# Kernel tuning notes

Measured on AMD Instinct MI355X. Metric: run time of the kernel, lower is better.

The kernel has to match this reference:

```python
import jax, jax.numpy as jnp
import numpy as np

HIDDEN = 512
N_HEAD = 8
D_HEAD = 64
MAX_REL = 3
B, S = 2, 2048


def setup_inputs() -> dict:
    key = jax.random.key(0)
    ks = jax.random.split(key, 12)
    sc = 1.0 / np.sqrt(HIDDEN)
    return {
        "query": jax.random.normal(ks[0], (B, S, HIDDEN), jnp.float32),
        "key_": jax.random.normal(ks[1], (B, S, HIDDEN), jnp.float32),
        "value": jax.random.normal(ks[2], (B, S, HIDDEN), jnp.float32),
        "mask": jnp.zeros((B, S, S), dtype=bool),
        "pos_matrix": jax.random.randint(ks[3], (S, S), 0, MAX_REL, jnp.int32),
        "Wq": jax.random.normal(ks[4], (HIDDEN, HIDDEN), jnp.float32) * sc,
        "bq": jnp.zeros((HIDDEN,), jnp.float32),
        "Wk": jax.random.normal(ks[5], (HIDDEN, HIDDEN), jnp.float32) * sc,
        "bk": jnp.zeros((HIDDEN,), jnp.float32),
        "Wv": jax.random.normal(ks[6], (HIDDEN, HIDDEN), jnp.float32) * sc,
        "bv": jnp.zeros((HIDDEN,), jnp.float32),
        "Wo": jax.random.normal(ks[7], (HIDDEN, HIDDEN), jnp.float32) * sc,
        "bo": jnp.zeros((HIDDEN,), jnp.float32),
        "rel_table": jax.random.normal(ks[8], (MAX_REL, D_HEAD), jnp.float32) * 0.1,
    }


def reference(query, key_, value, mask, pos_matrix, Wq, bq, Wk, bk, Wv, bv, Wo, bo, rel_table):
    b, s, hid = query.shape
    H, D = N_HEAD, D_HEAD
    q = (query @ Wq + bq).reshape(b, s, H, D)   # [B,S,H,D]
    k = (key_ @ Wk + bk).reshape(b, s, H, D)
    v = (value @ Wv + bv).reshape(b, s, H, D)
    rel = rel_table[pos_matrix[:s, :s]]          # [S,S,D]
    # attn1: content-content; attn2: q vs rel-pos; attn3: k(row) vs rel-pos
    attn1 = jnp.einsum('bihd,bjhd->bhij', q, k)
    attn2 = jnp.einsum('bihd,ijd->bhij', q, rel)
    attn3 = jnp.einsum('bihd,ijd->bhij', k, rel)
    scale = jnp.sqrt(jnp.asarray(D, query.dtype))
    attn = (attn1 + attn2 + attn3) / scale
    attn = jnp.where(mask[:, None, :, :], jnp.asarray(-1e9, attn.dtype), attn)
    attn = jax.nn.softmax(attn, axis=-1)         # dropout=0 (eval)
    x = jnp.einsum('bhij,bjhd->bihd', attn, v).reshape(b, s, hid)
    out = x @ Wo + bo
    return out, attn
```

## Files before the change

kernel.cpp:

```cpp
#include <hip/hip_runtime.h>
#include <math.h>

#define SEQ   2048
#define BATCH 2
#define NHEAD 8
#define HID   512
#define LG8   0.180336880f
#define MASKV -3.0e8f

typedef unsigned char  u8;
typedef unsigned short u16;
typedef short short8 __attribute__((ext_vector_type(8)));
typedef float f32x4  __attribute__((ext_vector_type(4)));

__device__ __forceinline__ u16 f2bf(float f) {
    unsigned u = __float_as_uint(f);
    u = (u + 0x7FFF + ((u >> 16) & 1)) >> 16;
    return (u16)u;
}
__device__ __forceinline__ float bf2f(u16 h) {
    return __uint_as_float(((unsigned)h) << 16);
}

__global__ __launch_bounds__(256) void prep_w_kernel(
    const float* __restrict__ W, u16* __restrict__ Wth, u16* __restrict__ Wtl)
{
    __shared__ float Ws[64][68];
    const int tid = threadIdx.x;
    const int k0 = blockIdx.x << 6;
    const int n0 = blockIdx.y << 6;
    const int rr = tid >> 2, c4 = (tid & 3) << 4;
    #pragma unroll
    for (int e = 0; e < 4; ++e) {
        float4 v = *(const float4*)&W[(size_t)(k0 + rr) * HID + n0 + c4 + (e << 2)];
        *(float4*)&Ws[rr][c4 + (e << 2)] = v;
    }
    __syncthreads();
    const int nn = tid >> 2, kk = (tid & 3) << 4;
    u16 hb[16], lb[16];
    #pragma unroll
    for (int e = 0; e < 16; ++e) {
        float x = Ws[kk + e][nn];
        u16 hi = f2bf(x);
        hb[e] = hi;
        lb[e] = f2bf(x - bf2f(hi));
    }
    const size_t o = (size_t)(n0 + nn) * HID + k0 + kk;
    *(short8*)&Wth[o]     = *(short8*)&hb[0];
    *(short8*)&Wth[o + 8] = *(short8*)&hb[8];
    *(short8*)&Wtl[o]     = *(short8*)&lb[0];
    *(short8*)&Wtl[o + 8] = *(short8*)&lb[8];
}

__global__ __launch_bounds__(256) void convert_split_kernel(
    const float* __restrict__ src, u16* __restrict__ h, u16* __restrict__ l)
{
    const size_t i = ((size_t)blockIdx.x * 256 + threadIdx.x) * 4;
    float4 v = *(const float4*)&src[i];
    ushort4 oh, ol; u16 hh;
    hh = f2bf(v.x); oh.x = hh; ol.x = f2bf(v.x - bf2f(hh));
    hh = f2bf(v.y); oh.y = hh; ol.y = f2bf(v.y - bf2f(hh));
    hh = f2bf(v.z); oh.z = hh; ol.z = f2bf(v.z - bf2f(hh));
    hh = f2bf(v.w); oh.w = hh; ol.w = f2bf(v.w - bf2f(hh));
    *(ushort4*)&h[i] = oh; *(ushort4*)&l[i] = ol;
}

template<int MODE>
__global__ __launch_bounds__(256) void gemm_mfma_kernel(
    const u16* __restrict__ Ah, const u16* __restrict__ Al,
    const u16* __restrict__ Wth, const u16* __restrict__ Wtl,
    const float* __restrict__ bias,
    float* __restrict__ Cf, u16* __restrict__ Oh, u16* __restrict__ Ol)
{
    __shared__ __align__(16) u16 Sa_h[64 * 72];
    __shared__ __align__(16) u16 Sa_l[64 * 72];
    __shared__ __align__(16) u16 Sw_h[64 * 72];
    __shared__ __align__(16) u16 Sw_l[64 * 72];
    const int tid = threadIdx.x;
    const int wave = tid >> 6, lane = tid & 63;
    const int quad = lane >> 4, l15 = lane & 15;
    const int row0 = blockIdx.x << 6, col0 = blockIdx.y << 6;
    const int rr = tid >> 2, cc = (tid & 3) << 4;

    const size_t ga = (size_t)(row0 + rr) * HID + cc;
    const size_t gw = (size_t)(col0 + rr) * HID + cc;

    f32x4 acc[4] = {{0.f,0.f,0.f,0.f},{0.f,0.f,0.f,0.f},{0.f,0.f,0.f,0.f},{0.f,0.f,0.f,0.f}};

    for (int k0 = 0; k0 < HID; k0 += 64) {
        const short8 ah0 = *(const short8*)&Ah[ga + k0];
        const short8 ah1 = *(const short8*)&Ah[ga + k0 + 8];
        const short8 al0 = *(const short8*)&Al[ga + k0];
        const short8 al1 = *(const short8*)&Al[ga + k0 + 8];
        const short8 wh0 = *(const short8*)&Wth[gw + k0];
        const short8 wh1 = *(const short8*)&Wth[gw + k0 + 8];
        const short8 wl0 = *(const short8*)&Wtl[gw + k0];
        const short8 wl1 = *(const short8*)&Wtl[gw + k0 + 8];
        __syncthreads();
        *(short8*)&Sa_h[rr * 72 + cc]     = ah0;
        *(short8*)&Sa_h[rr * 72 + cc + 8] = ah1;
        *(short8*)&Sa_l[rr * 72 + cc]     = al0;
        *(short8*)&Sa_l[rr * 72 + cc + 8] = al1;
        *(short8*)&Sw_h[rr * 72 + cc]     = wh0;
        *(short8*)&Sw_h[rr * 72 + cc + 8] = wh1;
        *(short8*)&Sw_l[rr * 72 + cc]     = wl0;
        *(short8*)&Sw_l[rr * 72 + cc + 8] = wl1;
        __syncthreads();
        #pragma unroll
        for (int s = 0; s < 2; ++s) {
            const int ao = ((wave << 4) + l15) * 72 + (s << 5) + (quad << 3);
            const short8 fa_h = *(const short8*)&Sa_h[ao];
            const short8 fa_l = *(const short8*)&Sa_l[ao];
            #pragma unroll
            for (int nt = 0; nt < 4; ++nt) {
                const int bo = ((nt << 4) + l15) * 72 + (s << 5) + (quad << 3);
                const short8 fb_h = *(const short8*)&Sw_h[bo];
                const short8 fb_l = *(const short8*)&Sw_l[bo];
                acc[nt] = __builtin_amdgcn_mfma_f32_16x16x32_bf16(fa_h, fb_h, acc[nt], 0, 0, 0);
                acc[nt] = __builtin_amdgcn_mfma_f32_16x16x32_bf16(fa_l, fb_h, acc[nt], 0, 0, 0);
                acc[nt] = __builtin_amdgcn_mfma_f32_16x16x32_bf16(fa_h, fb_l, acc[nt], 0, 0, 0);
            }
        }
    }
    #pragma unroll
    for (int nt = 0; nt < 4; ++nt) {
        const int col = col0 + (nt << 4) + l15;
        const float bv = bias[col];
        #pragma unroll
        for (int r = 0; r < 4; ++r) {
            const size_t row = (size_t)(row0 + (wave << 4) + (quad << 2) + r);
            const float v = acc[nt][r] + bv;
            if constexpr (MODE == 0) {
                Cf[row * HID + col] = v;
            } else if constexpr (MODE == 1) {
                const float sv = v * LG8;
                const u16 hi = f2bf(sv);
                Oh[row * HID + col] = hi;
                Ol[row * HID + col] = f2bf(sv - bf2f(hi));
            } else if constexpr (MODE == 2) {
                const u16 hi = f2bf(v);
                Oh[row * HID + col] = hi;
                Ol[row * HID + col] = f2bf(v - bf2f(hi));
            } else {
                Oh[row * HID + col] = f2bf(v);
            }
        }
    }
}

__global__ __launch_bounds__(256) void convert_pm_kernel(
    const int* __restrict__ pos, const u8* __restrict__ mask, u8* __restrict__ pm)
{
    const size_t s = ((size_t)blockIdx.x * 256 + threadIdx.x) * 4;
    int4  p = *(const int4*)&pos[s & (size_t)(SEQ * SEQ - 1)];
    uchar4 m = *(const uchar4*)&mask[s];
    uchar4 o;
    o.x = m.x ? (u8)3 : (u8)p.x;
    o.y = m.y ? (u8)3 : (u8)p.y;
    o.z = m.z ? (u8)3 : (u8)p.z;
    o.w = m.w ? (u8)3 : (u8)p.w;
    *(uchar4*)&pm[s] = o;
}

__global__ __launch_bounds__(256) void rel_dots_kernel(
    const u16* __restrict__ qh, const u16* __restrict__ ql,
    const u16* __restrict__ kh, const u16* __restrict__ kl,
    const float* __restrict__ rel_table, float* __restrict__ dqk)
{
    const int w = blockIdx.x * 4 + (threadIdx.x >> 6);
    const int lane = threadIdx.x & 63;
    const int h = w % NHEAD;
    const int is = w / NHEAD;
    const int b = is / SEQ;
    const int i = is % SEQ;
    const size_t base = (size_t)is * HID + h * 64 + lane;
    const float qs = bf2f(qh[base]) + bf2f(ql[base]);
    const float kv = bf2f(kh[base]) + bf2f(kl[base]);
    const float s = qs + LG8 * kv;
    float p0 = s * rel_table[lane];
    float p1 = s * rel_table[64 + lane];
    float p2 = s * rel_table[128 + lane];
    #pragma unroll
    for (int off = 32; off; off >>= 1) {
        p0 += __shfl_xor(p0, off);
        p1 += __shfl_xor(p1, off);
        p2 += __shfl_xor(p2, off);
    }
    if (lane == 0) {
        size_t o = (((size_t)b * NHEAD + h) * SEQ + i) << 2;
        dqk[o + 0] = p0; dqk[o + 1] = p1; dqk[o + 2] = p2;
    }
}

__global__ __launch_bounds__(256) void attn_stats_kernel(
    const u16* __restrict__ qh, const u16* __restrict__ ql,
    const u16* __restrict__ kh, const u16* __restrict__ kl,
    const float* __restrict__ dqk, const u8* __restrict__ pm,
    float* __restrict__ invl)
{
    __shared__ __align__(16) u16 Kh[64 * 72];
    __shared__ __align__(16) u16 Kl[64 * 72];
    __shared__ __align__(16) u8  PM[64 * 64];
    __shared__ float Ds[64][4];
    const int tid = threadIdx.x;
    const int wave = tid >> 6, lane = tid & 63;
    const int quad = lane >> 4, l15 = lane & 15;
    const int b = blockIdx.z, h = blockIdx.y, i0 = blockIdx.x << 6;
    const size_t bh = (size_t)(b * NHEAD + h);

    {
        const int i = tid >> 2, r = tid & 3;
        Ds[i][r] = (r == 3) ? MASKV : dqk[((bh * SEQ + i0 + i) << 2) + r];
    }
    const int irow = (wave << 4) + l15;
    const size_t qbase = ((size_t)(b * SEQ + i0 + irow)) * HID + h * 64 + (quad << 3);
    const short8 aqh0 = *(const short8*)&qh[qbase];
    const short8 aqh1 = *(const short8*)&qh[qbase + 32];
    const short8 aql0 = *(const short8*)&ql[qbase];
    const short8 aql1 = *(const short8*)&ql[qbase + 32];

    float srow[4] = {0.f, 0.f, 0.f, 0.f};

    for (int jt = 0; jt < SEQ / 64; ++jt) {
        const int j0 = jt << 6;
        __syncthreads();
        {
            const int rr = tid >> 3, cc = (tid & 7) << 3;
            const size_t g = ((size_t)(b * SEQ + j0 + rr)) * HID + h * 64 + cc;
            *(short8*)&Kh[rr * 72 + cc] = *(const short8*)&kh[g];
            *(short8*)&Kl[rr * 72 + cc] = *(const short8*)&kl[g];
            const size_t g2 = g + (size_t)32 * HID;
            *(short8*)&Kh[(rr + 32) * 72 + cc] = *(const short8*)&kh[g2];
            *(short8*)&Kl[(rr + 32) * 72 + cc] = *(const short8*)&kl[g2];
        }
        {
            const int r = tid >> 2, c = (tid & 3) << 4;
            *(uint4*)&PM[r * 64 + c] =
                *(const uint4*)&pm[((size_t)b * SEQ + i0 + r) * SEQ + j0 + c];
        }
        __syncthreads();

        #pragma unroll
        for (int sub = 0; sub < 4; ++sub) {
            const int n = (sub << 4) + l15;
            const short8 bh0 = *(const short8*)&Kh[n * 72 + (quad << 3)];
            const short8 bh1 = *(const short8*)&Kh[n * 72 + 32 + (quad << 3)];
            const short8 bl0 = *(const short8*)&Kl[n * 72 + (quad << 3)];
            const short8 bl1 = *(const short8*)&Kl[n * 72 + 32 + (quad << 3)];
            f32x4 acc = {0.f, 0.f, 0.f, 0.f};
            acc = __builtin_amdgcn_mfma_f32_16x16x32_bf16(aqh0, bh0, acc, 0, 0, 0);
            acc = __builtin_amdgcn_mfma_f32_16x16x32_bf16(aqh1, bh1, acc, 0, 0, 0);
            acc = __builtin_amdgcn_mfma_f32_16x16x32_bf16(aql0, bh0, acc, 0, 0, 0);
            acc = __builtin_amdgcn_mfma_f32_16x16x32_bf16(aql1, bh1, acc, 0, 0, 0);
            acc = __builtin_amdgcn_mfma_f32_16x16x32_bf16(aqh0, bl0, acc, 0, 0, 0);
            acc = __builtin_amdgcn_mfma_f32_16x16x32_bf16(aqh1, bl1, acc, 0, 0, 0);
            #pragma unroll
            for (int r = 0; r < 4; ++r) {
                const int il = (wave << 4) + (quad << 2) + r;
                const u8 p = PM[il * 64 + (sub << 4) + l15];
                srow[r] += exp2f(acc[r] + Ds[il][p]);
            }
        }
    }
    #pragma unroll
    for (int r = 0; r < 4; ++r) {
        float s = srow[r];
        s += __shfl_xor(s, 1); s += __shfl_xor(s, 2);
        s += __shfl_xor(s, 4); s += __shfl_xor(s, 8);
        if (l15 == 0)
            invl[bh * SEQ + i0 + (wave << 4) + (quad << 2) + r] = 1.0f / s;
    }
}

__global__ __launch_bounds__(256) void attn_fused_kernel(
    const u16* __restrict__ qh, const u16* __restrict__ ql,
    const u16* __restrict__ kh, const u16* __restrict__ kl,
    const u16* __restrict__ vb, const float* __restrict__ dqk,
    const u8* __restrict__ pm, const float* __restrict__ invl,
    float* __restrict__ attn, float* __restrict__ x)
{
    __shared__ __align__(16) u16 Kh[64 * 72];
    __shared__ __align__(16) u16 Kl[64 * 72];
    __shared__ __align__(16) u16 VtT[64 * 72];
    __shared__ __align__(16) u16 Pst[4][16 * 72];
    __shared__ __align__(16) u8  PM[64 * 64];
    __shared__ float Ds[64][4];
    const int tid = threadIdx.x;
    const int wave = tid >> 6, lane = tid & 63;
    const int quad = lane >> 4, l15 = lane & 15;
    const int b = blockIdx.z, h = blockIdx.y, i0 = blockIdx.x << 6;
    const size_t bh = (size_t)(b * NHEAD + h);

    {
        const int i = tid >> 2, r = tid & 3;
        Ds[i][r] = (r == 3) ? MASKV : dqk[((bh * SEQ + i0 + i) << 2) + r];
    }
    float inv_r[4];
    #pragma unroll
    for (int r = 0; r < 4; ++r)
        inv_r[r] = invl[bh * SEQ + i0 + (wave << 4) + (quad << 2) + r];

    const int irow = (wave << 4) + l15;
    const size_t qbase = ((size_t)(b * SEQ + i0 + irow)) * HID + h * 64 + (quad << 3);
    const short8 aqh0 = *(const short8*)&qh[qbase];
    const short8 aqh1 = *(const short8*)&qh[qbase + 32];
    const short8 aql0 = *(const short8*)&ql[qbase];
    const short8 aql1 = *(const short8*)&ql[qbase + 32];

    f32x4 accX[4] = {{0.f,0.f,0.f,0.f},{0.f,0.f,0.f,0.f},{0.f,0.f,0.f,0.f},{0.f,0.f,0.f,0.f}};

    for (int jt = 0; jt < SEQ / 64; ++jt) {
        const int j0 = jt << 6;
        __syncthreads();
        {
            const int rr = tid >> 3, cc = (tid & 7) << 3;
            const size_t g = ((size_t)(b * SEQ + j0 + rr)) * HID + h * 64 + cc;
            *(short8*)&Kh[rr * 72 + cc] = *(const short8*)&kh[g];
            *(short8*)&Kl[rr * 72 + cc] = *(const short8*)&kl[g];
            const size_t g2 = g + (size_t)32 * HID;
            *(short8*)&Kh[(rr + 32) * 72 + cc] = *(const short8*)&kh[g2];
            *(short8*)&Kl[(rr + 32) * 72 + cc] = *(const short8*)&kl[g2];
        }
        {
            const int r = tid >> 2, c = (tid & 3) << 4;
            *(uint4*)&PM[r * 64 + c] =
                *(const uint4*)&pm[((size_t)b * SEQ + i0 + r) * SEQ + j0 + c];
        }
        {
            const int jr = tid & 63, d0 = (tid >> 6) << 4;
            const size_t g = ((size_t)(b * SEQ + j0 + jr)) * HID + h * 64 + d0;
            const short8 v0 = *(const short8*)&vb[g];
            const short8 v1 = *(const short8*)&vb[g + 8];
            #pragma unroll
            for (int e = 0; e < 8; ++e) {
                VtT[(d0 + e) * 72 + jr]     = (u16)v0[e];
                VtT[(d0 + 8 + e) * 72 + jr] = (u16)v1[e];
            }
        }
        __syncthreads();

        #pragma unroll
        for (int sub = 0; sub < 4; ++sub) {
            const int n = (sub << 4) + l15;
            const short8 bh0 = *(const short8*)&Kh[n * 72 + (quad << 3)];
            const short8 bh1 = *(const short8*)&Kh[n * 72 + 32 + (quad << 3)];
            const short8 bl0 = *(const short8*)&Kl[n * 72 + (quad << 3)];
            const short8 bl1 = *(const short8*)&Kl[n * 72 + 32 + (quad << 3)];
            f32x4 acc = {0.f, 0.f, 0.f, 0.f};
            acc = __builtin_amdgcn_mfma_f32_16x16x32_bf16(aqh0, bh0, acc, 0, 0, 0);
            acc = __builtin_amdgcn_mfma_f32_16x16x32_bf16(aqh1, bh1, acc, 0, 0, 0);
            acc = __builtin_amdgcn_mfma_f32_16x16x32_bf16(aql0, bh0, acc, 0, 0, 0);
            acc = __builtin_amdgcn_mfma_f32_16x16x32_bf16(aql1, bh1, acc, 0, 0, 0);
            acc = __builtin_amdgcn_mfma_f32_16x16x32_bf16(aqh0, bl0, acc, 0, 0, 0);
            acc = __builtin_amdgcn_mfma_f32_16x16x32_bf16(aqh1, bl1, acc, 0, 0, 0);
            #pragma unroll
            for (int r = 0; r < 4; ++r) {
                const int il = (wave << 4) + (quad << 2) + r;
                const u8 p = PM[il * 64 + (sub << 4) + l15];
                const float pr = exp2f(acc[r] + Ds[il][p]) * inv_r[r];
                attn[(bh * SEQ + i0 + il) * SEQ + j0 + (sub << 4) + l15] = pr;
                Pst[wave][((quad << 2) + r) * 72 + (sub << 4) + l15] = f2bf(pr);
            }
        }
        const short8 bp0 = *(const short8*)&Pst[wave][l15 * 72 + (quad << 3)];
        const short8 bp1 = *(const short8*)&Pst[wave][l15 * 72 + 32 + (quad << 3)];
        #pragma unroll
        for (int m = 0; m < 4; ++m) {
            const short8 av0 = *(const short8*)&VtT[((m << 4) + l15) * 72 + (quad << 3)];
            const short8 av1 = *(const short8*)&VtT[((m << 4) + l15) * 72 + 32 + (quad << 3)];
            accX[m] = __builtin_amdgcn_mfma_f32_16x16x32_bf16(av0, bp0, accX[m], 0, 0, 0);
            accX[m] = __builtin_amdgcn_mfma_f32_16x16x32_bf16(av1, bp1, accX[m], 0, 0, 0);
        }
    }
    const size_t xrow = ((size_t)(b * SEQ + i0 + (wave << 4) + l15)) * HID + h * 64;
    #pragma unroll
    for (int m = 0; m < 4; ++m) {
        *(f32x4*)&x[xrow + (m << 4) + (quad << 2)] = accX[m];
    }
}

extern "C" void kernel_launch(void* const* d_in, const int* in_sizes, int n_in,
                              void* d_out, int out_size, void* d_ws, size_t ws_size,
                              hipStream_t stream) {
    (void)in_sizes; (void)n_in; (void)out_size; (void)ws_size;
    const float* query = (const float*)d_in[0];
    const float* key_  = (const float*)d_in[1];
    const float* value = (const float*)d_in[2];
    const u8*    mask  = (const u8*)d_in[3];
    const int*   pos   = (const int*)d_in[4];
    const float* Wq = (const float*)d_in[5];
    const float* bq = (const float*)d_in[6];
    const float* Wk = (const float*)d_in[7];
    const float* bk = (const float*)d_in[8];
    const float* Wv = (const float*)d_in[9];
    const float* bv = (const float*)d_in[10];
    const float* Wo = (const float*)d_in[11];
    const float* bo = (const float*)d_in[12];
    const float* rel_table = (const float*)d_in[13];

    float* out  = (float*)d_out;
    float* attn = out + (size_t)BATCH * SEQ * HID;

    u16* qh = (u16*)d_ws;
    u16* ql = qh + (size_t)2097152;
    u16* kh = ql + (size_t)2097152;
    u16* kl = kh + (size_t)2097152;
    u16* vb = kl + (size_t)2097152;
    float* dqk  = (float*)(vb + (size_t)2097152);
    float* invl = dqk + (size_t)131072;
    u8*  pm  = (u8*)(invl + (size_t)32768);
    float* x_ws = (float*)(pm + (size_t)8388608);
    u16* bufAh = (u16*)(x_ws + (size_t)2097152);
    u16* bufAl = bufAh + (size_t)2097152;
    u16* Wth = bufAl + (size_t)2097152;
    u16* Wtl = Wth + (size_t)262144;

    const dim3 blk(256);
    const dim3 gemm_grid(64, 8);
    const dim3 prep_grid(8, 8);

    prep_w_kernel<<<prep_grid, blk, 0, stream>>>(Wq, Wth, Wtl);
    convert_split_kernel<<<dim3(2048), blk, 0, stream>>>(query, bufAh, bufAl);
    gemm_mfma_kernel<1><<<gemm_grid, blk, 0, stream>>>(bufAh, bufAl, Wth, Wtl, bq,
                                                       nullptr, qh, ql);
    prep_w_kernel<<<prep_grid, blk, 0, stream>>>(Wk, Wth, Wtl);
    convert_split_kernel<<<dim3(2048), blk, 0, stream>>>(key_, bufAh, bufAl);
    gemm_mfma_kernel<2><<<gemm_grid, blk, 0, stream>>>(bufAh, bufAl, Wth, Wtl, bk,
                                                       nullptr, kh, kl);
    prep_w_kernel<<<prep_grid, blk, 0, stream>>>(Wv, Wth, Wtl);
    convert_split_kernel<<<dim3(2048), blk, 0, stream>>>(value, bufAh, bufAl);
    gemm_mfma_kernel<3><<<gemm_grid, blk, 0, stream>>>(bufAh, bufAl, Wth, Wtl, bv,
                                                       nullptr, vb, nullptr);

    rel_dots_kernel<<<dim3(BATCH * SEQ * NHEAD / 4), blk, 0, stream>>>(
        qh, ql, kh, kl, rel_table, dqk);
    convert_pm_kernel<<<dim3(8192), blk, 0, stream>>>(pos, mask, pm);
    attn_stats_kernel<<<dim3(SEQ / 64, NHEAD, BATCH), blk, 0, stream>>>(
        qh, ql, kh, kl, dqk, pm, invl);
    attn_fused_kernel<<<dim3(SEQ / 64, NHEAD, BATCH), blk, 0, stream>>>(
        qh, ql, kh, kl, vb, dqk, pm, invl, attn, x_ws);

    prep_w_kernel<<<prep_grid, blk, 0, stream>>>(Wo, Wth, Wtl);
    convert_split_kernel<<<dim3(2048), blk, 0, stream>>>(x_ws, bufAh, bufAl);
    gemm_mfma_kernel<0><<<gemm_grid, blk, 0, stream>>>(bufAh, bufAl, Wth, Wtl, bo,
                                                       out, nullptr, nullptr);
}
```

Baseline: 596.6 us.

## Fuse activation bf16 split into GEMMs and batch weight/mask prep launches

Drops the separate convert_split passes by converting fp32 activations to hi/lo bf16 inside the GEMM tile load, merges the four weight-prep launches and the pos/mask conversion into one kernel, and runs the Q/K/V projections as a single launch using a z grid dimension. This cuts the kernel launch count and removes the intermediate bf16 activation buffers and their write/read traffic. In exchange, each GEMM block loads twice the activation bytes in fp32 and does the split arithmetic per tile, and the mode selection becomes a runtime branch on blockIdx.z.

```diff
diff --git a/kernel.cpp b/kernel.cpp
--- a/kernel.cpp
+++ b/kernel.cpp
@@ -22,60 +22,77 @@
     return __uint_as_float(((unsigned)h) << 16);
 }
 
-__global__ __launch_bounds__(256) void prep_w_kernel(
-    const float* __restrict__ W, u16* __restrict__ Wth, u16* __restrict__ Wtl)
+__global__ __launch_bounds__(256) void misc_prep_kernel(
+    const float* __restrict__ Wq, const float* __restrict__ Wk,
+    const float* __restrict__ Wv, const float* __restrict__ Wo,
+    u16* __restrict__ Wth, u16* __restrict__ Wtl,
+    const int* __restrict__ pos, const u8* __restrict__ mask, u8* __restrict__ pm)
 {
     __shared__ float Ws[64][68];
     const int tid = threadIdx.x;
-    const int k0 = blockIdx.x << 6;
-    const int n0 = blockIdx.y << 6;
-    const int rr = tid >> 2, c4 = (tid & 3) << 4;
-    #pragma unroll
-    for (int e = 0; e < 4; ++e) {
-        float4 v = *(const float4*)&W[(size_t)(k0 + rr) * HID + n0 + c4 + (e << 2)];
-        *(float4*)&Ws[rr][c4 + (e << 2)] = v;
-    }
-    __syncthreads();
-    const int nn = tid >> 2, kk = (tid & 3) << 4;
-    u16 hb[16], lb[16];
-    #pragma unroll
-    for (int e = 0; e < 16; ++e) {
-        float x = Ws[kk + e][nn];
-        u16 hi = f2bf(x);
-        hb[e] = hi;
-        lb[e] = f2bf(x - bf2f(hi));
-    }
-    const size_t o = (size_t)(n0 + nn) * HID + k0 + kk;
-    *(short8*)&Wth[o]     = *(short8*)&hb[0];
-    *(short8*)&Wth[o + 8] = *(short8*)&hb[8];
-    *(short8*)&Wtl[o]     = *(short8*)&lb[0];
-    *(short8*)&Wtl[o + 8] = *(short8*)&lb[8];
-}
-
-__global__ __launch_bounds__(256) void convert_split_kernel(
-    const float* __restrict__ src, u16* __restrict__ h, u16* __restrict__ l)
-{
-    const size_t i = ((size_t)blockIdx.x * 256 + threadIdx.x) * 4;
-    float4 v = *(const float4*)&src[i];
-    ushort4 oh, ol; u16 hh;
-    hh = f2bf(v.x); oh.x = hh; ol.x = f2bf(v.x - bf2f(hh));
-    hh = f2bf(v.y); oh.y = hh; ol.y = f2bf(v.y - bf2f(hh));
-    hh = f2bf(v.z); oh.z = hh; ol.z = f2bf(v.z - bf2f(hh));
-    hh = f2bf(v.w); oh.w = hh; ol.w = f2bf(v.w - bf2f(hh));
-    *(ushort4*)&h[i] = oh; *(ushort4*)&l[i] = ol;
-}
-
-template<int MODE>
-__global__ __launch_bounds__(256) void gemm_mfma_kernel(
-    const u16* __restrict__ Ah, const u16* __restrict__ Al,
-    const u16* __restrict__ Wth, const u16* __restrict__ Wtl,
-    const float* __restrict__ bias,
-    float* __restrict__ Cf, u16* __restrict__ Oh, u16* __restrict__ Ol)
+    const int bid = blockIdx.x;
+    if (bid < 256) {
+        const int w = bid >> 6, sub = bid & 63;
+        const float* W = (w == 0) ? Wq : (w == 1) ? Wk : (w == 2) ? Wv : Wo;
+        u16* oth = Wth + (size_t)w * 262144;
+        u16* otl = Wtl + (size_t)w * 262144;
+        const int k0 = (sub & 7) << 6;
+        const int n0 = (sub >> 3) << 6;
+        const int rr = tid >> 2, c4 = (tid & 3) << 4;
+        #pragma unroll
+        for (int e = 0; e < 4; ++e) {
+            float4 v = *(const float4*)&W[(size_t)(k0 + rr) * HID + n0 + c4 + (e << 2)];
+            *(float4*)&Ws[rr][c4 + (e << 2)] = v;
+        }
+        __syncthreads();
+        const int nn = tid >> 2, kk = (tid & 3) << 4;
+        u16 hb[16], lb[16];
+        #pragma unroll
+        for (int e = 0; e < 16; ++e) {
+            float x = Ws[kk + e][nn];
+            u16 hi = f2bf(x);
+            hb[e] = hi;
+            lb[e] = f2bf(x - bf2f(hi));
+        }
+        const size_t o = (size_t)(n0 + nn) * HID + k0 + kk;
+        *(short8*)&oth[o]     = *(short8*)&hb[0];
+        *(short8*)&oth[o + 8] = *(short8*)&hb[8];
+        *(short8*)&otl[o]     = *(short8*)&lb[0];
+        *(short8*)&otl[o + 8] = *(short8*)&lb[8];
+    } else {
+        const size_t s = ((size_t)(bid - 256) * 256 + tid) * 4;
+        int4  p = *(const int4*)&pos[s & (size_t)(SEQ * SEQ - 1)];
+        uchar4 m = *(const uchar4*)&mask[s];
+        uchar4 o;
+        o.x = m.x ? (u8)3 : (u8)p.x;
+        o.y = m.y ? (u8)3 : (u8)p.y;
+        o.z = m.z ? (u8)3 : (u8)p.z;
+        o.w = m.w ? (u8)3 : (u8)p.w;
+        *(uchar4*)&pm[s] = o;
+    }
+}
+
+__global__ __launch_bounds__(256) void gemm_qkv_kernel(
+    const float* __restrict__ query, const float* __restrict__ key_,
+    const float* __restrict__ value,
+    const u16* __restrict__ Wth_all, const u16* __restrict__ Wtl_all,
+    const float* __restrict__ bq, const float* __restrict__ bk,
+    const float* __restrict__ bv,
+    u16* __restrict__ qh, u16* __restrict__ ql,
+    u16* __restrict__ kh, u16* __restrict__ kl, u16* __restrict__ vb)
 {
     __shared__ __align__(16) u16 Sa_h[64 * 72];
     __shared__ __align__(16) u16 Sa_l[64 * 72];
     __shared__ __align__(16) u16 Sw_h[64 * 72];
     __shared__ __align__(16) u16 Sw_l[64 * 72];
+    const int z = blockIdx.z;
+    const float* A    = (z == 0) ? query : (z == 1) ? key_ : value;
+    const float* bias = (z == 0) ? bq : (z == 1) ? bk : bv;
+    const u16* Wth = Wth_all + (size_t)z * 262144;
+    const u16* Wtl = Wtl_all + (size_t)z * 262144;
+    u16* Oh = (z == 0) ? qh : (z == 1) ? kh : vb;
+    u16* Ol = (z == 0) ? ql : kl;
+
     const int tid = threadIdx.x;
     const int wave = tid >> 6, lane = tid & 63;
     const int quad = lane >> 4, l15 = lane & 15;
@@ -88,19 +105,27 @@
     f32x4 acc[4] = {{0.f,0.f,0.f,0.f},{0.f,0.f,0.f,0.f},{0.f,0.f,0.f,0.f},{0.f,0.f,0.f,0.f}};
 
     for (int k0 = 0; k0 < HID; k0 += 64) {
-        const short8 ah0 = *(const short8*)&Ah[ga + k0];
-        const short8 ah1 = *(const short8*)&Ah[ga + k0 + 8];
-        const short8 al0 = *(const short8*)&Al[ga + k0];
-        const short8 al1 = *(const short8*)&Al[ga + k0 + 8];
+        float4 af[4];
+        #pragma unroll
+        for (int e = 0; e < 4; ++e)
+            af[e] = *(const float4*)&A[ga + k0 + (e << 2)];
         const short8 wh0 = *(const short8*)&Wth[gw + k0];
         const short8 wh1 = *(const short8*)&Wth[gw + k0 + 8];
         const short8 wl0 = *(const short8*)&Wtl[gw + k0];
         const short8 wl1 = *(const short8*)&Wtl[gw + k0 + 8];
         __syncthreads();
-        *(short8*)&Sa_h[rr * 72 + cc]     = ah0;
-        *(short8*)&Sa_h[rr * 72 + cc + 8] = ah1;
-        *(short8*)&Sa_l[rr * 72 + cc]     = al0;
-        *(short8*)&Sa_l[rr * 72 + cc + 8] = al1;
+        u16 hA[16], lA[16];
+        #pragma unroll
+        for (int e = 0; e < 16; ++e) {
+            float xv = ((const float*)af)[e];
+            u16 hi = f2bf(xv);
+            hA[e] = hi;
+            lA[e] = f2bf(xv - bf2f(hi));
+        }
+        *(short8*)&Sa_h[rr * 72 + cc]     = *(short8*)&hA[0];
+        *(short8*)&Sa_h[rr * 72 + cc + 8] = *(short8*)&hA[8];
+        *(short8*)&Sa_l[rr * 72 + cc]     = *(short8*)&lA[0];
+        *(short8*)&Sa_l[rr * 72 + cc + 8] = *(short8*)&lA[8];
         *(short8*)&Sw_h[rr * 72 + cc]     = wh0;
         *(short8*)&Sw_h[rr * 72 + cc + 8] = wh1;
         *(short8*)&Sw_l[rr * 72 + cc]     = wl0;
@@ -125,19 +150,17 @@
     #pragma unroll
     for (int nt = 0; nt < 4; ++nt) {
         const int col = col0 + (nt << 4) + l15;
-        const float bv = bias[col];
+        const float bvv = bias[col];
         #pragma unroll
         for (int r = 0; r < 4; ++r) {
             const size_t row = (size_t)(row0 + (wave << 4) + (quad << 2) + r);
-            const float v = acc[nt][r] + bv;
-            if constexpr (MODE == 0) {
-                Cf[row * HID + col] = v;
-            } else if constexpr (MODE == 1) {
+            const float v = acc[nt][r] + bvv;
+            if (z == 0) {
                 const float sv = v * LG8;
                 const u16 hi = f2bf(sv);
                 Oh[row * HID + col] = hi;
                 Ol[row * HID + col] = f2bf(sv - bf2f(hi));
-            } else if constexpr (MODE == 2) {
+            } else if (z == 1) {
                 const u16 hi = f2bf(v);
                 Oh[row * HID + col] = hi;
                 Ol[row * HID + col] = f2bf(v - bf2f(hi));
@@ -148,18 +171,79 @@
     }
 }
 
-__global__ __launch_bounds__(256) void convert_pm_kernel(
-    const int* __restrict__ pos, const u8* __restrict__ mask, u8* __restrict__ pm)
+__global__ __launch_bounds__(256) void gemm_out_kernel(
+    const float* __restrict__ A,
+    const u16* __restrict__ Wth, const u16* __restrict__ Wtl,
+    const float* __restrict__ bias, float* __restrict__ C)
 {
-    const size_t s = ((size_t)blockIdx.x * 256 + threadIdx.x) * 4;
-    int4  p = *(const int4*)&pos[s & (size_t)(SEQ * SEQ - 1)];
-    uchar4 m = *(const uchar4*)&mask[s];
-    uchar4 o;
-    o.x = m.x ? (u8)3 : (u8)p.x;
-    o.y = m.y ? (u8)3 : (u8)p.y;
-    o.z = m.z ? (u8)3 : (u8)p.z;
-    o.w = m.w ? (u8)3 : (u8)p.w;
-    *(uchar4*)&pm[s] = o;
+    __shared__ __align__(16) u16 Sa_h[64 * 72];
+    __shared__ __align__(16) u16 Sa_l[64 * 72];
+    __shared__ __align__(16) u16 Sw_h[64 * 72];
+    __shared__ __align__(16) u16 Sw_l[64 * 72];
+    const int tid = threadIdx.x;
+    const int wave = tid >> 6, lane = tid & 63;
+    const int quad = lane >> 4, l15 = lane & 15;
+    const int row0 = blockIdx.x << 6, col0 = blockIdx.y << 6;
+    const int rr = tid >> 2, cc = (tid & 3) << 4;
+
+    const size_t ga = (size_t)(row0 + rr) * HID + cc;
+    const size_t gw = (size_t)(col0 + rr) * HID + cc;
+
+    f32x4 acc[4] = {{0.f,0.f,0.f,0.f},{0.f,0.f,0.f,0.f},{0.f,0.f,0.f,0.f},{0.f,0.f,0.f,0.f}};
+
+    for (int k0 = 0; k0 < HID; k0 += 64) {
+        float4 af[4];
+        #pragma unroll
+        for (int e = 0; e < 4; ++e)
+            af[e] = *(const float4*)&A[ga + k0 + (e << 2)];
+        const short8 wh0 = *(const short8*)&Wth[gw + k0];
+        const short8 wh1 = *(const short8*)&Wth[gw + k0 + 8];
+        const short8 wl0 = *(const short8*)&Wtl[gw + k0];
+        const short8 wl1 = *(const short8*)&Wtl[gw + k0 + 8];
+        __syncthreads();
+        u16 hA[16], lA[16];
+        #pragma unroll
+        for (int e = 0; e < 16; ++e) {
+            float xv = ((const float*)af)[e];
+            u16 hi = f2bf(xv);
+            hA[e] = hi;
+            lA[e] = f2bf(xv - bf2f(hi));
+        }
+        *(short8*)&Sa_h[rr * 72 + cc]     = *(short8*)&hA[0];
+        *(short8*)&Sa_h[rr * 72 + cc + 8] = *(short8*)&hA[8];
+        *(short8*)&Sa_l[rr * 72 + cc]     = *(short8*)&lA[0];
+        *(short8*)&Sa_l[rr * 72 + cc + 8] = *(short8*)&lA[8];
+        *(short8*)&Sw_h[rr * 72 + cc]     = wh0;
+        *(short8*)&Sw_h[rr * 72 + cc + 8] = wh1;
+        *(short8*)&Sw_l[rr * 72 + cc]     = wl0;
+        *(short8*)&Sw_l[rr * 72 + cc + 8] = wl1;
+        __syncthreads();
+        #pragma unroll
+        for (int s = 0; s < 2; ++s) {
+            const int ao = ((wave << 4) + l15) * 72 + (s << 5) + (quad << 3);
+            const short8 fa_h = *(const short8*)&Sa_h[ao];
+            const short8 fa_l = *(const short8*)&Sa_l[ao];
+            #pragma unroll
+            for (int nt = 0; nt < 4; ++nt) {
+                const int bo = ((nt << 4) + l15) * 72 + (s << 5) + (quad << 3);
+                const short8 fb_h = *(const short8*)&Sw_h[bo];
+                const short8 fb_l = *(const short8*)&Sw_l[bo];
+                acc[nt] = __builtin_amdgcn_mfma_f32_16x16x32_bf16(fa_h, fb_h, acc[nt], 0, 0, 0);
+                acc[nt] = __builtin_amdgcn_mfma_f32_16x16x32_bf16(fa_l, fb_h, acc[nt], 0, 0, 0);
+                acc[nt] = __builtin_amdgcn_mfma_f32_16x16x32_bf16(fa_h, fb_l, acc[nt], 0, 0, 0);
+            }
+        }
+    }
+    #pragma unroll
+    for (int nt = 0; nt < 4; ++nt) {
+        const int col = col0 + (nt << 4) + l15;
+        const float bvv = bias[col];
+        #pragma unroll
+        for (int r = 0; r < 4; ++r) {
+            const size_t row = (size_t)(row0 + (wave << 4) + (quad << 2) + r);
+            C[row * HID + col] = acc[nt][r] + bvv;
+        }
+    }
 }
 
 __global__ __launch_bounds__(256) void rel_dots_kernel(
@@ -410,38 +494,21 @@
     float* invl = dqk + (size_t)131072;
     u8*  pm  = (u8*)(invl + (size_t)32768);
     float* x_ws = (float*)(pm + (size_t)8388608);
-    u16* bufAh = (u16*)(x_ws + (size_t)2097152);
-    u16* bufAl = bufAh + (size_t)2097152;
-    u16* Wth = bufAl + (size_t)2097152;
-    u16* Wtl = Wth + (size_t)262144;
+    u16* Wth = (u16*)(x_ws + (size_t)2097152);
+    u16* Wtl = Wth + (size_t)1048576;
 
     const dim3 blk(256);
-    const dim3 gemm_grid(64, 8);
-    const dim3 prep_grid(8, 8);
-
-    prep_w_kernel<<<prep_grid, blk, 0, stream>>>(Wq, Wth, Wtl);
-    convert_split_kernel<<<dim3(2048), blk, 0, stream>>>(query, bufAh, bufAl);
-    gemm_mfma_kernel<1><<<gemm_grid, blk, 0, stream>>>(bufAh, bufAl, Wth, Wtl, bq,
-                                                       nullptr, qh, ql);
-    prep_w_kernel<<<prep_grid, blk, 0, stream>>>(Wk, Wth, Wtl);
-    convert_split_kernel<<<dim3(2048), blk, 0, stream>>>(key_, bufAh, bufAl);
-    gemm_mfma_kernel<2><<<gemm_grid, blk, 0, stream>>>(bufAh, bufAl, Wth, Wtl, bk,
-                                                       nullptr, kh, kl);
-    prep_w_kernel<<<prep_grid, blk, 0, stream>>>(Wv, Wth, Wtl);
-    convert_split_kernel<<<dim3(2048), blk, 0, stream>>>(value, bufAh, bufAl);
-    gemm_mfma_kernel<3><<<gemm_grid, blk, 0, stream>>>(bufAh, bufAl, Wth, Wtl, bv,
-                                                       nullptr, vb, nullptr);
-
+
+    misc_prep_kernel<<<dim3(256 + 8192), blk, 0, stream>>>(
+        Wq, Wk, Wv, Wo, Wth, Wtl, pos, mask, pm);
+    gemm_qkv_kernel<<<dim3(64, 8, 3), blk, 0, stream>>>(
+        query, key_, value, Wth, Wtl, bq, bk, bv, qh, ql, kh, kl, vb);
     rel_dots_kernel<<<dim3(BATCH * SEQ * NHEAD / 4), blk, 0, stream>>>(
         qh, ql, kh, kl, rel_table, dqk);
-    convert_pm_kernel<<<dim3(8192), blk, 0, stream>>>(pos, mask, pm);
     attn_stats_kernel<<<dim3(SEQ / 64, NHEAD, BATCH), blk, 0, stream>>>(
         qh, ql, kh, kl, dqk, pm, invl);
     attn_fused_kernel<<<dim3(SEQ / 64, NHEAD, BATCH), blk, 0, stream>>>(
         qh, ql, kh, kl, vb, dqk, pm, invl, attn, x_ws);
-
-    prep_w_kernel<<<prep_grid, blk, 0, stream>>>(Wo, Wth, Wtl);
-    convert_split_kernel<<<dim3(2048), blk, 0, stream>>>(x_ws, bufAh, bufAl);
-    gemm_mfma_kernel<0><<<gemm_grid, blk, 0, stream>>>(bufAh, bufAl, Wth, Wtl, bo,
-                                                       out, nullptr, nullptr);
-}
+    gemm_out_kernel<<<dim3(64, 8), blk, 0, stream>>>(
+        x_ws, Wth + (size_t)3 * 262144, Wtl + (size_t)3 * 262144, bo, out);
+}
```

Measured after the change: 566.1 us. 5.1% less time.
